# Performance work log

Measured on AMD Instinct MI355X. Metric: run time of the kernel, lower is better.

## Reference

```python
import jax, jax.numpy as jnp
import numpy as np

CDIM = 256  # part_size for energy_pooling_mask


def setup_inputs() -> dict:
    key = jax.random.key(0)
    ks = jax.random.split(key, 6)
    B, T, IDIM, HDIM, ODIM = 8, 2048, 512, 2048, 512
    x = jax.random.normal(ks[0], (B, T, IDIM), dtype=jnp.float32)
    mask_prev = jax.random.randint(ks[1], (B, T, HDIM), 0, 2, dtype=jnp.int32)
    W_enc = jax.random.normal(ks[2], (HDIM, IDIM), dtype=jnp.float32) * 0.02
    b_enc = jax.random.normal(ks[3], (HDIM,), dtype=jnp.float32) * 0.02
    W_dec = jax.random.normal(ks[4], (ODIM, HDIM), dtype=jnp.float32) * 0.02
    b_dec = jax.random.normal(ks[5], (ODIM,), dtype=jnp.float32) * 0.02
    return {"x": x, "mask_prev": mask_prev, "W_enc": W_enc, "b_enc": b_enc,
            "W_dec": W_dec, "b_dec": b_dec}


def _energy_pooling_mask(h, part_size):
    # topk over channel (last) dim of h^2; share=True -> k = 2*part_size
    B, T, H = h.shape
    k2 = 2 * part_size
    _, idx = jax.lax.top_k(h * h, k2)            # [B, T, 2c] unique indices
    idx_f = idx.reshape(B * T, k2)
    rows = jnp.arange(B * T)[:, None]
    base = jnp.zeros((B * T, H), dtype=h.dtype)
    # sum of one-hots over unique indices == scatter-set of 1.0
    mask_share = base.at[rows, idx_f].set(1.0).reshape(B, T, H)
    mask_cur = base.at[rows, idx_f[:, :part_size]].set(1.0).reshape(B, T, H)
    return mask_cur, mask_share


def reference(x, mask_prev, W_enc, b_enc, W_dec, b_dec):
    # encoder: Linear(idim -> hdim)
    h = jnp.einsum('bti,hi->bth', x, W_enc) + b_enc
    # hidden_exclude_activation with mask_prev given:
    # h[mask_prev.bool()] = 0
    mp = mask_prev.astype(h.dtype)
    h = jnp.where(mp > 0, jnp.zeros((), h.dtype), h)
    mask_cur, mask_cur_share = _energy_pooling_mask(h, CDIM)
    mask_prev_new = mp + mask_cur
    # h.masked_fill(~mask_cur_share.bool(), 0)
    h = h * mask_cur_share
    # decoder_src: Linear(hdim -> odim)
    out = jnp.einsum('bth,oh->bto', h, W_dec) + b_dec
    return out, mask_prev_new
```

## Files before the change

### kernel.cpp

```cpp
#include <hip/hip_runtime.h>
#include <hip/hip_bf16.h>

typedef __attribute__((ext_vector_type(8))) __bf16 bf16x8;
typedef __attribute__((ext_vector_type(4))) float f32x4;

#define MDIM 16384
#define HDIM 2048
#define IDIM 512
#define ODIM 512

static __device__ __forceinline__ unsigned short f2bf(float f) {
  unsigned int u = __float_as_uint(f);
  unsigned int r = (u + 0x7fffu + ((u >> 16) & 1u)) >> 16;
  return (unsigned short)r;
}

__global__ void cvt_bf16_kernel(const float* __restrict__ src,
                                unsigned short* __restrict__ dst, int n) {
  int i = (blockIdx.x * 256 + threadIdx.x) * 4;
  if (i >= n) return;
  float4 v = *(const float4*)(src + i);
  unsigned int a = (unsigned int)f2bf(v.x) | ((unsigned int)f2bf(v.y) << 16);
  unsigned int b = (unsigned int)f2bf(v.z) | ((unsigned int)f2bf(v.w) << 16);
  uint2 st; st.x = a; st.y = b;
  *(uint2*)(dst + i) = st;
}

__global__ __launch_bounds__(256) void gemm1_kernel(
    const float* __restrict__ x,
    const float* __restrict__ wenc,
    const float* __restrict__ benc,
    const int* __restrict__ maskp,
    float* __restrict__ h) {
  __shared__ __align__(16) float As[16][132];
  __shared__ __align__(16) float Bs[16][132];
  const int t = threadIdx.x;
  const int tx = t & 15, ty = t >> 4;
  const int m0 = blockIdx.y * 128;
  const int n0 = blockIdx.x * 128;
  const int r0 = t >> 2;
  const int k4 = (t & 3) * 4;

  const float* pa0 = x + (size_t)(m0 + r0) * IDIM + k4;
  const float* pa1 = x + (size_t)(m0 + 64 + r0) * IDIM + k4;
  const float* pb0 = wenc + (size_t)(n0 + r0) * IDIM + k4;
  const float* pb1 = wenc + (size_t)(n0 + 64 + r0) * IDIM + k4;

  float acc[8][8];
#pragma unroll
  for (int i = 0; i < 8; ++i)
#pragma unroll
    for (int j = 0; j < 8; ++j) acc[i][j] = 0.f;

  for (int kt = 0; kt < IDIM; kt += 16) {
    float4 a0 = *(const float4*)(pa0 + kt);
    float4 a1 = *(const float4*)(pa1 + kt);
    float4 b0 = *(const float4*)(pb0 + kt);
    float4 b1 = *(const float4*)(pb1 + kt);
    __syncthreads();
#pragma unroll
    for (int j = 0; j < 4; ++j) {
      As[k4 + j][r0]      = ((const float*)&a0)[j];
      As[k4 + j][64 + r0] = ((const float*)&a1)[j];
      Bs[k4 + j][r0]      = ((const float*)&b0)[j];
      Bs[k4 + j][64 + r0] = ((const float*)&b1)[j];
    }
    __syncthreads();
#pragma unroll
    for (int k = 0; k < 16; ++k) {
      float4 av0 = *(const float4*)&As[k][ty * 4];
      float4 av1 = *(const float4*)&As[k][64 + ty * 4];
      float4 bv0 = *(const float4*)&Bs[k][tx * 4];
      float4 bv1 = *(const float4*)&Bs[k][64 + tx * 4];
      float am[8] = {av0.x, av0.y, av0.z, av0.w, av1.x, av1.y, av1.z, av1.w};
      float bm[8] = {bv0.x, bv0.y, bv0.z, bv0.w, bv1.x, bv1.y, bv1.z, bv1.w};
#pragma unroll
      for (int i = 0; i < 8; ++i)
#pragma unroll
        for (int j = 0; j < 8; ++j) acc[i][j] += am[i] * bm[j];
    }
  }
  float4 be0 = *(const float4*)(benc + n0 + tx * 4);
  float4 be1 = *(const float4*)(benc + n0 + 64 + tx * 4);
  float bb[8] = {be0.x, be0.y, be0.z, be0.w, be1.x, be1.y, be1.z, be1.w};
#pragma unroll
  for (int i = 0; i < 8; ++i) {
    int m = m0 + ((i < 4) ? (ty * 4 + i) : (64 + ty * 4 + (i - 4)));
    const int* mrow = maskp + (size_t)m * HDIM + n0;
    int4 mk0 = *(const int4*)(mrow + tx * 4);
    int4 mk1 = *(const int4*)(mrow + 64 + tx * 4);
    int mm[8] = {mk0.x, mk0.y, mk0.z, mk0.w, mk1.x, mk1.y, mk1.z, mk1.w};
    float o[8];
#pragma unroll
    for (int j = 0; j < 8; ++j) {
      float v = acc[i][j] + bb[j];
      o[j] = (mm[j] > 0) ? 0.f : v;
    }
    float* hrow = h + (size_t)m * HDIM + n0;
    float4 s0 = {o[0], o[1], o[2], o[3]};
    float4 s1 = {o[4], o[5], o[6], o[7]};
    *(float4*)(hrow + tx * 4) = s0;
    *(float4*)(hrow + 64 + tx * 4) = s1;
  }
}

__global__ __launch_bounds__(256) void select_kernel(
    float* __restrict__ hbuf,
    const int* __restrict__ maskp,
    unsigned short* __restrict__ hs) {
  const int row = blockIdx.x;
  const int t = threadIdx.x;
  const int lane = t & 63;
  const int w = t >> 6;
  __shared__ int red[4];

  float* hrow = hbuf + (size_t)row * HDIM;
  float hv[8];
  *(float4*)&hv[0] = *(const float4*)(hrow + t * 8);
  *(float4*)&hv[4] = *(const float4*)(hrow + t * 8 + 4);
  unsigned int key[8];
#pragma unroll
  for (int i = 0; i < 8; ++i) key[i] = __float_as_uint(hv[i] * hv[i]);

  unsigned int v512 = 0, v256 = 0;
  for (int b = 31; b >= 0; --b) {
    unsigned int c1 = v512 | (1u << b);
    unsigned int c2 = v256 | (1u << b);
    int cnt = 0;
#pragma unroll
    for (int i = 0; i < 8; ++i) {
      cnt += (key[i] >= c1) ? 1 : 0;
      cnt += (key[i] >= c2) ? (1 << 16) : 0;
    }
#pragma unroll
    for (int d = 1; d < 64; d <<= 1) cnt += __shfl_xor(cnt, d, 64);
    if (lane == 0) red[w] = cnt;
    __syncthreads();
    int tot = red[0] + red[1] + red[2] + red[3];
    __syncthreads();
    if ((tot & 0xffff) >= 512) v512 = c1;
    if ((tot >> 16) >= 256) v256 = c2;
  }
  int g = 0;
#pragma unroll
  for (int i = 0; i < 8; ++i) {
    g += (key[i] > v512) ? 1 : 0;
    g += (key[i] > v256) ? (1 << 16) : 0;
  }
#pragma unroll
  for (int d = 1; d < 64; d <<= 1) g += __shfl_xor(g, d, 64);
  if (lane == 0) red[w] = g;
  __syncthreads();
  g = red[0] + red[1] + red[2] + red[3];
  __syncthreads();
  const int r512 = 512 - (g & 0xffff);
  const int r256 = 256 - (g >> 16);

  int tc = 0;
#pragma unroll
  for (int i = 0; i < 8; ++i) {
    tc += (key[i] == v512) ? 1 : 0;
    tc += (key[i] == v256) ? (1 << 16) : 0;
  }
  int sc = tc;
#pragma unroll
  for (int d = 1; d < 64; d <<= 1) {
    int o = __shfl_up(sc, d, 64);
    if (lane >= d) sc += o;
  }
  if (lane == 63) red[w] = sc;
  __syncthreads();
  int excl = sc - tc;
  for (int i = 0; i < w; ++i) excl += red[i];
  int run512 = excl & 0xffff;
  int run256 = (excl >> 16) & 0xffff;

  const int* mrow = maskp + (size_t)row * HDIM;
  int4 mp0 = *(const int4*)(mrow + t * 8);
  int4 mp1 = *(const int4*)(mrow + t * 8 + 4);
  int mm[8] = {mp0.x, mp0.y, mp0.z, mp0.w, mp1.x, mp1.y, mp1.z, mp1.w};

  float mpn[8];
  unsigned int hb[4];
#pragma unroll
  for (int i = 0; i < 8; ++i) {
    bool share, cur;
    if (key[i] > v512) share = true;
    else if (key[i] == v512) { share = (run512 < r512); run512++; }
    else share = false;
    if (key[i] > v256) cur = true;
    else if (key[i] == v256) { cur = (run256 < r256); run256++; }
    else cur = false;
    mpn[i] = (float)mm[i] + (cur ? 1.0f : 0.0f);
    unsigned short bbits = f2bf(share ? hv[i] : 0.0f);
    if (i & 1) hb[i >> 1] |= ((unsigned int)bbits << 16);
    else hb[i >> 1] = (unsigned int)bbits;
  }
  float4 s0 = {mpn[0], mpn[1], mpn[2], mpn[3]};
  float4 s1 = {mpn[4], mpn[5], mpn[6], mpn[7]};
  *(float4*)(hrow + t * 8) = s0;
  *(float4*)(hrow + t * 8 + 4) = s1;
  uint4 hstore = {hb[0], hb[1], hb[2], hb[3]};
  *(uint4*)(hs + (size_t)row * HDIM + t * 8) = hstore;
}

__global__ __launch_bounds__(256) void gemm2_kernel(
    const unsigned short* __restrict__ A,
    const unsigned short* __restrict__ B,
    const float* __restrict__ bdec,
    float* __restrict__ out) {
  __shared__ __align__(16) __bf16 As[128 * 32];
  __shared__ __align__(16) __bf16 Bs[128 * 32];
  const int t = threadIdx.x;
  const int lane = t & 63;
  const int w = t >> 6;
  const int wm = w >> 1, wn = w & 1;
  const int m0 = blockIdx.y * 128;
  const int n0 = blockIdx.x * 128;
  const int r = t >> 2;
  const int k8 = (t & 3) * 8;

  f32x4 acc[4][4];
#pragma unroll
  for (int i = 0; i < 4; ++i)
#pragma unroll
    for (int j = 0; j < 4; ++j) acc[i][j] = (f32x4){0.f, 0.f, 0.f, 0.f};

  const int la = lane & 15;
  const int kq = (lane >> 4) * 8;

  for (int kt = 0; kt < HDIM; kt += 32) {
    uint4 a0 = *(const uint4*)(A + (size_t)(m0 + r) * HDIM + kt + k8);
    uint4 a1 = *(const uint4*)(A + (size_t)(m0 + 64 + r) * HDIM + kt + k8);
    uint4 b0 = *(const uint4*)(B + (size_t)(n0 + r) * HDIM + kt + k8);
    uint4 b1 = *(const uint4*)(B + (size_t)(n0 + 64 + r) * HDIM + kt + k8);
    __syncthreads();
    *(uint4*)&As[r * 32 + k8] = a0;
    *(uint4*)&As[(64 + r) * 32 + k8] = a1;
    *(uint4*)&Bs[r * 32 + k8] = b0;
    *(uint4*)&Bs[(64 + r) * 32 + k8] = b1;
    __syncthreads();
    bf16x8 af[4], bg[4];
#pragma unroll
    for (int mi = 0; mi < 4; ++mi)
      af[mi] = *(const bf16x8*)&As[(wm * 64 + mi * 16 + la) * 32 + kq];
#pragma unroll
    for (int ni = 0; ni < 4; ++ni)
      bg[ni] = *(const bf16x8*)&Bs[(wn * 64 + ni * 16 + la) * 32 + kq];
#pragma unroll
    for (int mi = 0; mi < 4; ++mi)
#pragma unroll
      for (int ni = 0; ni < 4; ++ni)
        acc[mi][ni] = __builtin_amdgcn_mfma_f32_16x16x32_bf16(
            af[mi], bg[ni], acc[mi][ni], 0, 0, 0);
  }
  const int rq = (lane >> 4) * 4;
#pragma unroll
  for (int mi = 0; mi < 4; ++mi) {
#pragma unroll
    for (int ni = 0; ni < 4; ++ni) {
      int n = n0 + wn * 64 + ni * 16 + la;
      float bd = bdec[n];
#pragma unroll
      for (int rr = 0; rr < 4; ++rr) {
        int m = m0 + wm * 64 + mi * 16 + rq + rr;
        out[(size_t)m * ODIM + n] = acc[mi][ni][rr] + bd;
      }
    }
  }
}

extern "C" void kernel_launch(void* const* d_in, const int* in_sizes, int n_in,
                              void* d_out, int out_size, void* d_ws, size_t ws_size,
                              hipStream_t stream) {
  const float* x = (const float*)d_in[0];
  const int* mask_prev = (const int*)d_in[1];
  const float* W_enc = (const float*)d_in[2];
  const float* b_enc = (const float*)d_in[3];
  const float* W_dec = (const float*)d_in[4];
  const float* b_dec = (const float*)d_in[5];

  float* out = (float*)d_out;
  float* hbuf = out + (size_t)MDIM * ODIM;
  unsigned short* hs = (unsigned short*)d_ws;
  unsigned short* wdec = hs + (size_t)MDIM * HDIM;

  cvt_bf16_kernel<<<dim3((ODIM * HDIM) / (256 * 4)), dim3(256), 0, stream>>>(
      W_dec, wdec, ODIM * HDIM);
  gemm1_kernel<<<dim3(HDIM / 128, MDIM / 128), dim3(256), 0, stream>>>(
      x, W_enc, b_enc, mask_prev, hbuf);
  select_kernel<<<dim3(MDIM), dim3(256), 0, stream>>>(hbuf, mask_prev, hs);
  gemm2_kernel<<<dim3(ODIM / 128, MDIM / 128), dim3(256), 0, stream>>>(
      hs, wdec, b_dec, out);
}
```

Baseline: 858.7 us.

## Use histogram radix select for top-k threshold and move mask into select

The 32-pass bitwise threshold search in the select kernel becomes a 4096-bin shared-memory histogram over the top key bits. A prefix scan then finds the threshold bins, and the few candidates in those bins are refined with a small per-wave bit search. This removes roughly 64 block-wide barriers per row. Applying mask_prev also moves from the first GEMM epilogue into the select kernel, so the large int mask is read once instead of twice. The first GEMM also gains register prefetch of the next k-tile. The candidate buffers are capped at 768 entries, so a bin that overflows that cap would give a wrong threshold.

```diff
diff --git a/kernel.cpp b/kernel.cpp
--- a/kernel.cpp
+++ b/kernel.cpp
@@ -8,6 +8,7 @@
 #define HDIM 2048
 #define IDIM 512
 #define ODIM 512
+#define CAP 768
 
 static __device__ __forceinline__ unsigned short f2bf(float f) {
   unsigned int u = __float_as_uint(f);
@@ -30,7 +31,6 @@
     const float* __restrict__ x,
     const float* __restrict__ wenc,
     const float* __restrict__ benc,
-    const int* __restrict__ maskp,
     float* __restrict__ h) {
   __shared__ __align__(16) float As[16][132];
   __shared__ __align__(16) float Bs[16][132];
@@ -52,11 +52,12 @@
 #pragma unroll
     for (int j = 0; j < 8; ++j) acc[i][j] = 0.f;
 
+  float4 a0 = *(const float4*)(pa0);
+  float4 a1 = *(const float4*)(pa1);
+  float4 b0 = *(const float4*)(pb0);
+  float4 b1 = *(const float4*)(pb1);
+
   for (int kt = 0; kt < IDIM; kt += 16) {
-    float4 a0 = *(const float4*)(pa0 + kt);
-    float4 a1 = *(const float4*)(pa1 + kt);
-    float4 b0 = *(const float4*)(pb0 + kt);
-    float4 b1 = *(const float4*)(pb1 + kt);
     __syncthreads();
 #pragma unroll
     for (int j = 0; j < 4; ++j) {
@@ -66,6 +67,12 @@
       Bs[k4 + j][64 + r0] = ((const float*)&b1)[j];
     }
     __syncthreads();
+    if (kt + 16 < IDIM) {
+      a0 = *(const float4*)(pa0 + kt + 16);
+      a1 = *(const float4*)(pa1 + kt + 16);
+      b0 = *(const float4*)(pb0 + kt + 16);
+      b1 = *(const float4*)(pb1 + kt + 16);
+    }
 #pragma unroll
     for (int k = 0; k < 16; ++k) {
       float4 av0 = *(const float4*)&As[k][ty * 4];
@@ -86,19 +93,9 @@
 #pragma unroll
   for (int i = 0; i < 8; ++i) {
     int m = m0 + ((i < 4) ? (ty * 4 + i) : (64 + ty * 4 + (i - 4)));
-    const int* mrow = maskp + (size_t)m * HDIM + n0;
-    int4 mk0 = *(const int4*)(mrow + tx * 4);
-    int4 mk1 = *(const int4*)(mrow + 64 + tx * 4);
-    int mm[8] = {mk0.x, mk0.y, mk0.z, mk0.w, mk1.x, mk1.y, mk1.z, mk1.w};
-    float o[8];
-#pragma unroll
-    for (int j = 0; j < 8; ++j) {
-      float v = acc[i][j] + bb[j];
-      o[j] = (mm[j] > 0) ? 0.f : v;
-    }
     float* hrow = h + (size_t)m * HDIM + n0;
-    float4 s0 = {o[0], o[1], o[2], o[3]};
-    float4 s1 = {o[4], o[5], o[6], o[7]};
+    float4 s0 = {acc[i][0] + bb[0], acc[i][1] + bb[1], acc[i][2] + bb[2], acc[i][3] + bb[3]};
+    float4 s1 = {acc[i][4] + bb[4], acc[i][5] + bb[5], acc[i][6] + bb[6], acc[i][7] + bb[7]};
     *(float4*)(hrow + tx * 4) = s0;
     *(float4*)(hrow + 64 + tx * 4) = s1;
   }
@@ -112,35 +109,102 @@
   const int t = threadIdx.x;
   const int lane = t & 63;
   const int w = t >> 6;
-  __shared__ int red[4];
+  __shared__ int hist[4096];
+  __shared__ unsigned int cand512[CAP];
+  __shared__ unsigned int cand256[CAP];
+  __shared__ int scal[16];
+  __shared__ int n512, n256;
 
   float* hrow = hbuf + (size_t)row * HDIM;
+  const int* mrow = maskp + (size_t)row * HDIM;
   float hv[8];
   *(float4*)&hv[0] = *(const float4*)(hrow + t * 8);
   *(float4*)&hv[4] = *(const float4*)(hrow + t * 8 + 4);
+  int4 mp0 = *(const int4*)(mrow + t * 8);
+  int4 mp1 = *(const int4*)(mrow + t * 8 + 4);
+  int mm[8] = {mp0.x, mp0.y, mp0.z, mp0.w, mp1.x, mp1.y, mp1.z, mp1.w};
+#pragma unroll
+  for (int i = 0; i < 8; ++i) hv[i] = (mm[i] > 0) ? 0.f : hv[i];
   unsigned int key[8];
 #pragma unroll
   for (int i = 0; i < 8; ++i) key[i] = __float_as_uint(hv[i] * hv[i]);
 
-  unsigned int v512 = 0, v256 = 0;
-  for (int b = 31; b >= 0; --b) {
-    unsigned int c1 = v512 | (1u << b);
-    unsigned int c2 = v256 | (1u << b);
-    int cnt = 0;
-#pragma unroll
-    for (int i = 0; i < 8; ++i) {
-      cnt += (key[i] >= c1) ? 1 : 0;
-      cnt += (key[i] >= c2) ? (1 << 16) : 0;
-    }
-#pragma unroll
-    for (int d = 1; d < 64; d <<= 1) cnt += __shfl_xor(cnt, d, 64);
-    if (lane == 0) red[w] = cnt;
-    __syncthreads();
-    int tot = red[0] + red[1] + red[2] + red[3];
-    __syncthreads();
-    if ((tot & 0xffff) >= 512) v512 = c1;
-    if ((tot >> 16) >= 256) v256 = c2;
-  }
+#pragma unroll
+  for (int i = 0; i < 16; ++i) hist[t + i * 256] = 0;
+  if (t == 0) {
+    n512 = 0; n256 = 0;
+    scal[0] = 0; scal[1] = 0x40000000;
+    scal[2] = 0; scal[3] = 0x40000000;
+  }
+  __syncthreads();
+#pragma unroll
+  for (int i = 0; i < 8; ++i)
+    if (key[i]) atomicAdd(&hist[key[i] >> 20], 1);
+  __syncthreads();
+
+  if (w == 0) {
+    const int base = lane * 64;
+    int s = 0;
+#pragma unroll
+    for (int i = 0; i < 64; i += 4) {
+      int4 hh = *(const int4*)&hist[base + i];
+      s += hh.x + hh.y + hh.z + hh.w;
+    }
+    int rs = s;
+#pragma unroll
+    for (int d = 1; d < 64; d <<= 1) {
+      int o = __shfl_down(rs, d, 64);
+      rs += (lane + d < 64) ? o : 0;
+    }
+    int c = rs - s;
+    for (int i = 60; i >= 0; i -= 4) {
+      int4 hh = *(const int4*)&hist[base + i];
+      int q[4] = {hh.x, hh.y, hh.z, hh.w};
+#pragma unroll
+      for (int j = 3; j >= 0; --j) {
+        int hc = q[j];
+        if (c < 512 && c + hc >= 512) { scal[0] = base + i + j; scal[1] = 512 - c; }
+        if (c < 256 && c + hc >= 256) { scal[2] = base + i + j; scal[3] = 256 - c; }
+        c += hc;
+      }
+    }
+  }
+  __syncthreads();
+  const int b512 = scal[0], b256 = scal[2];
+#pragma unroll
+  for (int i = 0; i < 8; ++i) {
+    if (key[i]) {
+      int bin = (int)(key[i] >> 20);
+      if (bin == b512) { int p = atomicAdd(&n512, 1); if (p < CAP) cand512[p] = key[i]; }
+      if (bin == b256) { int p = atomicAdd(&n256, 1); if (p < CAP) cand256[p] = key[i]; }
+    }
+  }
+  __syncthreads();
+
+  if (w < 2) {
+    const unsigned int bb = (unsigned int)scal[w * 2];
+    const int r = scal[w * 2 + 1];
+    const unsigned int* cand = w ? cand256 : cand512;
+    int C = w ? n256 : n512;
+    C = (C < CAP) ? C : CAP;
+    unsigned int v = 0;
+    if (r <= C) {
+      v = bb << 20;
+      for (int bit = 19; bit >= 0; --bit) {
+        unsigned int cth = v | (1u << bit);
+        int cnt = 0;
+        for (int p = lane; p < C; p += 64) cnt += (cand[p] >= cth) ? 1 : 0;
+#pragma unroll
+        for (int d = 1; d < 64; d <<= 1) cnt += __shfl_xor(cnt, d, 64);
+        if (cnt >= r) v = cth;
+      }
+    }
+    if (lane == 0) scal[4 + w] = (int)v;
+  }
+  __syncthreads();
+  const unsigned int v512 = (unsigned int)scal[4];
+  const unsigned int v256 = (unsigned int)scal[5];
+
   int g = 0;
 #pragma unroll
   for (int i = 0; i < 8; ++i) {
@@ -149,10 +213,9 @@
   }
 #pragma unroll
   for (int d = 1; d < 64; d <<= 1) g += __shfl_xor(g, d, 64);
-  if (lane == 0) red[w] = g;
-  __syncthreads();
-  g = red[0] + red[1] + red[2] + red[3];
-  __syncthreads();
+  if (lane == 0) scal[8 + w] = g;
+  __syncthreads();
+  g = scal[8] + scal[9] + scal[10] + scal[11];
   const int r512 = 512 - (g & 0xffff);
   const int r256 = 256 - (g >> 16);
 
@@ -168,17 +231,12 @@
     int o = __shfl_up(sc, d, 64);
     if (lane >= d) sc += o;
   }
-  if (lane == 63) red[w] = sc;
+  if (lane == 63) scal[12 + w] = sc;
   __syncthreads();
   int excl = sc - tc;
-  for (int i = 0; i < w; ++i) excl += red[i];
+  for (int i = 0; i < w; ++i) excl += scal[12 + i];
   int run512 = excl & 0xffff;
   int run256 = (excl >> 16) & 0xffff;
-
-  const int* mrow = maskp + (size_t)row * HDIM;
-  int4 mp0 = *(const int4*)(mrow + t * 8);
-  int4 mp1 = *(const int4*)(mrow + t * 8 + 4);
-  int mm[8] = {mp0.x, mp0.y, mp0.z, mp0.w, mp1.x, mp1.y, mp1.z, mp1.w};
 
   float mpn[8];
   unsigned int hb[4];
@@ -288,7 +346,7 @@
   cvt_bf16_kernel<<<dim3((ODIM * HDIM) / (256 * 4)), dim3(256), 0, stream>>>(
       W_dec, wdec, ODIM * HDIM);
   gemm1_kernel<<<dim3(HDIM / 128, MDIM / 128), dim3(256), 0, stream>>>(
-      x, W_enc, b_enc, mask_prev, hbuf);
+      x, W_enc, b_enc, hbuf);
   select_kernel<<<dim3(MDIM), dim3(256), 0, stream>>>(hbuf, mask_prev, hs);
   gemm2_kernel<<<dim3(ODIM / 128, MDIM / 128), dim3(256), 0, stream>>>(
       hs, wdec, b_dec, out);
```

Measured after the change: 855.9 us. About the same (-0.3%).
